# Kernel tuning notes

Measured on AMD Instinct MI355X. Metric: run time of the kernel, lower is better.

## Reference

```python
import jax, jax.numpy as jnp
import numpy as np

N = 4096
STD = 0.01


def setup_inputs() -> dict:
    key = jax.random.key(0)
    ks = jax.random.split(key, 16)
    p = lambda k, shape: STD * jax.random.normal(k, shape, dtype=jnp.float32)
    return {
        "t": 0,
        "x": jax.random.normal(ks[0], (N, 1), dtype=jnp.float32),
        "A": jax.random.normal(ks[1], (N, N), dtype=jnp.float32),
        # MLP_A: 2 -> 16 -> 16 -> 1 (ReLU between hidden layers), torch (out,in) layout
        "WA0": p(ks[2], (16, 2)), "bA0": p(ks[3], (16,)),
        "WA1": p(ks[4], (16, 16)), "bA1": p(ks[5], (16,)),
        "WA2": p(ks[6], (1, 16)), "bA2": p(ks[7], (1,)),
        # MLP: 1 -> 16 -> 1 (ReLU after first layer)
        "Wm0": p(ks[8], (16, 1)), "bm0": p(ks[9], (16,)),
        "Wm1": p(ks[10], (1, 16)), "bm1": p(ks[11], (1,)),
        # linear_A: 2 -> 1, no bias; linear_f: 1 -> 1, no bias
        "wA": p(ks[12], (1, 2)),
        "wf": p(ks[13], (1, 1)),
    }


def reference(t, x, A, WA0, bA0, WA1, bA1, WA2, bA2, Wm0, bm0, Wm1, bm1, wA, wf):
    n = x.shape[0]
    # node MLP branch: hidden_list[0] == 1 != 0
    x_N = jax.nn.relu(x @ Wm0.T + bm0) @ Wm1.T + bm1 + x @ wf.T  # (n, 1)
    # all-pairs features: x_a[i, j] = (x_i, x_j)
    x1 = jnp.broadcast_to(x, (n, n))       # row i = x_i repeated
    x2 = jnp.broadcast_to(x.T, (n, n))     # row i = full x vector
    x_a = jnp.stack((x1, x2), axis=-1)     # (n, n, 2)
    # edge MLP (2 -> 16 -> 16 -> 1) + skip linear_A (2 -> 1)
    h = jax.nn.relu(x_a @ WA0.T + bA0)     # (n, n, 16)
    h = jax.nn.relu(h @ WA1.T + bA1)       # (n, n, 16)
    x_e = (h @ WA2.T + bA2)[..., 0]        # (n, n)
    x_12 = (x_a @ wA.T)[..., 0]            # (n, n)
    # adjacency-weighted reduction over neighbors (dim=1)
    x_A = jnp.sum(A * (x_e + x_12), axis=1, keepdims=True)  # (n, 1)
    return x_N + x_A
```

## Files before the change

kernel.cpp:

```cpp
#include <hip/hip_runtime.h>
#include <hip/hip_bf16.h>


#define NN 4096

typedef __attribute__((ext_vector_type(8)))  short short8;
typedef __attribute__((ext_vector_type(2)))  float f32x2;
typedef __attribute__((ext_vector_type(16))) float f32x16;

__device__ __forceinline__ unsigned bf16_rne(float f) {
    unsigned u = __float_as_uint(f);
    return (u + 0x7fffu + ((u >> 16) & 1u)) >> 16;
}

__global__ __launch_bounds__(256, 4) void odef_kernel(
    const float* __restrict__ x,  const float* __restrict__ A,
    const float* __restrict__ WA0, const float* __restrict__ bA0,
    const float* __restrict__ WA1, const float* __restrict__ bA1,
    const float* __restrict__ WA2, const float* __restrict__ bA2,
    const float* __restrict__ Wm0, const float* __restrict__ bm0,
    const float* __restrict__ Wm1, const float* __restrict__ bm1,
    const float* __restrict__ wA,  const float* __restrict__ wf,
    float* __restrict__ out)
{
    __shared__ float partial[4];

    const int tid  = threadIdx.x;
    const int wave = tid >> 6;
    const int lane = tid & 63;
    const int n    = lane & 31;
    const int half = lane >> 5;
    const int row  = blockIdx.x * 2 + (wave >> 1);
    const int jbase = (wave & 1) * (NN / 2);

    const float xi = x[row];

    short8 a_frag;
    {
        union { short8 s8; unsigned u[4]; } au;
        #pragma unroll
        for (int p = 0; p < 4; ++p) {
            float lo = 0.f, hi = 0.f;
            if (n < 16) {
                int k = half * 8 + p * 2;
                lo = WA1[n * 16 + k];
                hi = WA1[n * 16 + k + 1];
            }
            au.u[p] = bf16_rne(lo) | (bf16_rne(hi) << 16);
        }
        a_frag = au.s8;
    }

    f32x2 u2[4], w2[4];
    #pragma unroll
    for (int p = 0; p < 4; ++p) {
        int k0 = half * 8 + p * 2;
        u2[p] = (f32x2){ fmaf(WA0[2 * k0],     xi, bA0[k0]),
                         fmaf(WA0[2 * k0 + 2], xi, bA0[k0 + 1]) };
        w2[p] = (f32x2){ WA0[2 * k0 + 1], WA0[2 * k0 + 3] };
    }

    f32x2 wa2_2[4];
    f32x16 cbias;
    #pragma unroll
    for (int r = 0; r < 16; ++r) cbias[r] = 0.f;
    #pragma unroll
    for (int q = 0; q < 4; ++q) {
        int r0 = 2 * q, r1 = 2 * q + 1;
        int m0 = (r0 & 3) + 8 * (r0 >> 2) + 4 * half;
        int m1 = (r1 & 3) + 8 * (r1 >> 2) + 4 * half;
        wa2_2[q] = (f32x2){ WA2[m0], WA2[m1] };
        cbias[r0] = bA1[m0];
        cbias[r1] = bA1[m1];
    }

    const float wA1h = half ? 0.f : wA[1];
    const float c0h  = half ? 0.f : (bA2[0] + wA[0] * xi);
    const f32x2 zero2 = { 0.f, 0.f };

    const float* Arow = A + (size_t)row * NN + jbase;
    const float* xrow = x + jbase;

    float acc = 0.f;

    #pragma unroll 2
    for (int jj = 0; jj < NN / 2; jj += 32) {
        float xg  = xrow[jj + n];
        float aij = Arow[jj + n];
        f32x2 xg2 = { xg, xg };
        union { short8 s8; unsigned u[4]; } bu;
        #pragma unroll
        for (int p = 0; p < 4; ++p) {
            f32x2 h = __builtin_elementwise_fma(w2[p], xg2, u2[p]);
            h = __builtin_elementwise_max(h, zero2);
            bu.u[p] = __builtin_amdgcn_perm(__float_as_uint(h.y),
                                            __float_as_uint(h.x),
                                            0x07060302u);
        }
        f32x16 d = __builtin_amdgcn_mfma_f32_32x32x16_bf16(a_frag, bu.s8, cbias, 0, 0, 0);
        f32x2 pp = { fmaf(wA1h, xg, c0h), 0.f };
        #pragma unroll
        for (int q = 0; q < 4; ++q) {
            f32x2 dq = { d[2 * q], d[2 * q + 1] };
            dq = __builtin_elementwise_max(dq, zero2);
            pp = __builtin_elementwise_fma(wa2_2[q], dq, pp);
        }
        acc = fmaf(aij, pp.x + pp.y, acc);
    }

    #pragma unroll
    for (int off = 32; off > 0; off >>= 1)
        acc += __shfl_xor(acc, off);
    if (lane == 0) partial[wave] = acc;
    __syncthreads();

    if (lane == 0 && (wave & 1) == 0) {
        float xn = fmaf(wf[0], xi, bm1[0]);
        #pragma unroll
        for (int h = 0; h < 16; ++h)
            xn = fmaf(Wm1[h], fmaxf(fmaf(Wm0[h], xi, bm0[h]), 0.f), xn);
        out[row] = xn + partial[wave] + partial[wave + 1];
    }
}

extern "C" void kernel_launch(void* const* d_in, const int* in_sizes, int n_in,
                              void* d_out, int out_size, void* d_ws, size_t ws_size,
                              hipStream_t stream) {
    const float* x   = (const float*)d_in[1];
    const float* A   = (const float*)d_in[2];
    const float* WA0 = (const float*)d_in[3];
    const float* bA0 = (const float*)d_in[4];
    const float* WA1 = (const float*)d_in[5];
    const float* bA1 = (const float*)d_in[6];
    const float* WA2 = (const float*)d_in[7];
    const float* bA2 = (const float*)d_in[8];
    const float* Wm0 = (const float*)d_in[9];
    const float* bm0 = (const float*)d_in[10];
    const float* Wm1 = (const float*)d_in[11];
    const float* bm1 = (const float*)d_in[12];
    const float* wA  = (const float*)d_in[13];
    const float* wf  = (const float*)d_in[14];
    float* out = (float*)d_out;

    odef_kernel<<<NN / 2, 256, 0, stream>>>(x, A, WA0, bA0, WA1, bA1, WA2, bA2,
                                            Wm0, bm0, Wm1, bm1, wA, wf, out);
}
```

Before: 168.9 us.

## Software-pipeline A and x loads with register double buffering and packed FMA asm

Result: faster. 163.4 us (-3.3%).

```diff
diff --git a/kernel.cpp b/kernel.cpp
--- a/kernel.cpp
+++ b/kernel.cpp
@@ -11,6 +11,15 @@
 __device__ __forceinline__ unsigned bf16_rne(float f) {
     unsigned u = __float_as_uint(f);
     return (u + 0x7fffu + ((u >> 16) & 1u)) >> 16;
+}
+
+__device__ __forceinline__ f32x2 pk_fma(f32x2 a, f32x2 b, f32x2 c) {
+    f32x2 d;
+    asm("v_pk_fma_f32 %0, %1, %2, %3" : "=v"(d) : "v"(a), "v"(b), "v"(c));
+    return d;
+}
+__device__ __forceinline__ f32x2 relu2(f32x2 a) {
+    return (f32x2){ fmaxf(a.x, 0.f), fmaxf(a.y, 0.f) };
 }
 
 __global__ __launch_bounds__(256, 4) void odef_kernel(
@@ -76,36 +85,49 @@
 
     const float wA1h = half ? 0.f : wA[1];
     const float c0h  = half ? 0.f : (bA2[0] + wA[0] * xi);
-    const f32x2 zero2 = { 0.f, 0.f };
 
     const float* Arow = A + (size_t)row * NN + jbase;
     const float* xrow = x + jbase;
 
     float acc = 0.f;
 
-    #pragma unroll 2
-    for (int jj = 0; jj < NN / 2; jj += 32) {
-        float xg  = xrow[jj + n];
-        float aij = Arow[jj + n];
-        f32x2 xg2 = { xg, xg };
-        union { short8 s8; unsigned u[4]; } bu;
+    float xb[2][8], ab[2][8];
+    #pragma unroll
+    for (int g = 0; g < 8; ++g) {
+        xb[0][g] = xrow[g * 32 + n];
+        ab[0][g] = Arow[g * 32 + n];
+    }
+
+    #pragma unroll
+    for (int m = 0; m < 8; ++m) {
+        const int cb = m & 1, nb = cb ^ 1;
+        const int mn = (m < 7) ? m + 1 : 7;
         #pragma unroll
-        for (int p = 0; p < 4; ++p) {
-            f32x2 h = __builtin_elementwise_fma(w2[p], xg2, u2[p]);
-            h = __builtin_elementwise_max(h, zero2);
-            bu.u[p] = __builtin_amdgcn_perm(__float_as_uint(h.y),
-                                            __float_as_uint(h.x),
-                                            0x07060302u);
+        for (int g = 0; g < 8; ++g) {
+            xb[nb][g] = xrow[mn * 256 + g * 32 + n];
+            ab[nb][g] = Arow[mn * 256 + g * 32 + n];
         }
-        f32x16 d = __builtin_amdgcn_mfma_f32_32x32x16_bf16(a_frag, bu.s8, cbias, 0, 0, 0);
-        f32x2 pp = { fmaf(wA1h, xg, c0h), 0.f };
         #pragma unroll
-        for (int q = 0; q < 4; ++q) {
-            f32x2 dq = { d[2 * q], d[2 * q + 1] };
-            dq = __builtin_elementwise_max(dq, zero2);
-            pp = __builtin_elementwise_fma(wa2_2[q], dq, pp);
+        for (int g = 0; g < 8; ++g) {
+            float xg  = xb[cb][g];
+            float aij = ab[cb][g];
+            f32x2 xg2 = { xg, xg };
+            union { short8 s8; unsigned u[4]; } bu;
+            #pragma unroll
+            for (int p = 0; p < 4; ++p) {
+                f32x2 h = relu2(pk_fma(w2[p], xg2, u2[p]));
+                bu.u[p] = __builtin_amdgcn_perm(__float_as_uint(h.y),
+                                                __float_as_uint(h.x),
+                                                0x07060302u);
+            }
+            union { f32x16 v16; f32x2 v2[8]; } du;
+            du.v16 = __builtin_amdgcn_mfma_f32_32x32x16_bf16(a_frag, bu.s8, cbias, 0, 0, 0);
+            f32x2 pp = { fmaf(wA1h, xg, c0h), 0.f };
+            #pragma unroll
+            for (int q = 0; q < 4; ++q)
+                pp = pk_fma(wa2_2[q], relu2(du.v2[q]), pp);
+            acc = fmaf(aij, pp.x + pp.y, acc);
         }
-        acc = fmaf(aij, pp.x + pp.y, acc);
     }
 
     #pragma unroll
```

## Switch edge MLP to fp16 packed math and prefetch inputs two iterations ahead

Applied to the files above, without the earlier changes.

Result: faster. 157.4 us (-6.8%).

```diff
diff --git a/kernel.cpp b/kernel.cpp
--- a/kernel.cpp
+++ b/kernel.cpp
@@ -4,13 +4,12 @@
 
 #define NN 4096
 
-typedef __attribute__((ext_vector_type(8)))  short short8;
-typedef __attribute__((ext_vector_type(2)))  float f32x2;
+typedef __fp16 half8  __attribute__((ext_vector_type(8)));
+typedef __fp16 half2v __attribute__((ext_vector_type(2)));
 typedef __attribute__((ext_vector_type(16))) float f32x16;
 
-__device__ __forceinline__ unsigned bf16_rne(float f) {
-    unsigned u = __float_as_uint(f);
-    return (u + 0x7fffu + ((u >> 16) & 1u)) >> 16;
+__device__ __forceinline__ half2v cvt2(float lo, float hi) {
+    return __builtin_amdgcn_cvt_pkrtz(lo, hi);
 }
 
 __global__ __launch_bounds__(256, 4) void odef_kernel(
@@ -35,77 +34,73 @@
 
     const float xi = x[row];
 
-    short8 a_frag;
-    {
-        union { short8 s8; unsigned u[4]; } au;
-        #pragma unroll
-        for (int p = 0; p < 4; ++p) {
-            float lo = 0.f, hi = 0.f;
-            if (n < 16) {
-                int k = half * 8 + p * 2;
-                lo = WA1[n * 16 + k];
-                hi = WA1[n * 16 + k + 1];
-            }
-            au.u[p] = bf16_rne(lo) | (bf16_rne(hi) << 16);
+    union { half2v h2[4]; half8 h8; } au;
+    #pragma unroll
+    for (int p = 0; p < 4; ++p) {
+        float lo = 0.f, hi = 0.f;
+        if (n < 16) {
+            int k = half * 8 + p * 2;
+            lo = WA1[n * 16 + k];
+            hi = WA1[n * 16 + k + 1];
         }
-        a_frag = au.s8;
+        au.h2[p] = cvt2(lo, hi);
     }
 
-    f32x2 u2[4], w2[4];
+    half2v u2h[4], w2h[4];
     #pragma unroll
     for (int p = 0; p < 4; ++p) {
         int k0 = half * 8 + p * 2;
-        u2[p] = (f32x2){ fmaf(WA0[2 * k0],     xi, bA0[k0]),
-                         fmaf(WA0[2 * k0 + 2], xi, bA0[k0 + 1]) };
-        w2[p] = (f32x2){ WA0[2 * k0 + 1], WA0[2 * k0 + 3] };
+        u2h[p] = cvt2(fmaf(WA0[2 * k0],     xi, bA0[k0]),
+                      fmaf(WA0[2 * k0 + 2], xi, bA0[k0 + 1]));
+        w2h[p] = cvt2(WA0[2 * k0 + 1], WA0[2 * k0 + 3]);
     }
 
-    f32x2 wa2_2[4];
+    float wa2s[8];
     f32x16 cbias;
     #pragma unroll
     for (int r = 0; r < 16; ++r) cbias[r] = 0.f;
     #pragma unroll
-    for (int q = 0; q < 4; ++q) {
-        int r0 = 2 * q, r1 = 2 * q + 1;
-        int m0 = (r0 & 3) + 8 * (r0 >> 2) + 4 * half;
-        int m1 = (r1 & 3) + 8 * (r1 >> 2) + 4 * half;
-        wa2_2[q] = (f32x2){ WA2[m0], WA2[m1] };
-        cbias[r0] = bA1[m0];
-        cbias[r1] = bA1[m1];
+    for (int r = 0; r < 8; ++r) {
+        int m = (r & 3) + 8 * (r >> 2) + 4 * half;
+        wa2s[r]  = WA2[m];
+        cbias[r] = bA1[m];
     }
 
     const float wA1h = half ? 0.f : wA[1];
     const float c0h  = half ? 0.f : (bA2[0] + wA[0] * xi);
-    const f32x2 zero2 = { 0.f, 0.f };
+    const half2v z2 = { (__fp16)0.f, (__fp16)0.f };
 
-    const float* Arow = A + (size_t)row * NN + jbase;
-    const float* xrow = x + jbase;
+    const float* xp = x + jbase;
+    const float* ap = A + (size_t)row * NN + jbase;
 
     float acc = 0.f;
 
-    #pragma unroll 2
-    for (int jj = 0; jj < NN / 2; jj += 32) {
-        float xg  = xrow[jj + n];
-        float aij = Arow[jj + n];
-        f32x2 xg2 = { xg, xg };
-        union { short8 s8; unsigned u[4]; } bu;
+    float xcur = xp[n],      acur = ap[n];
+    float xnxt = xp[32 + n], anxt = ap[32 + n];
+
+    #pragma unroll 4
+    for (int g = 0; g < 64; ++g) {
+        int gp = (g + 2 < 64) ? g + 2 : 63;
+        float xpre = xp[gp * 32 + n];
+        float apre = ap[gp * 32 + n];
+
+        half2v xgh = cvt2(xcur, xcur);
+        union { half2v h2[4]; half8 h8; } b;
         #pragma unroll
         for (int p = 0; p < 4; ++p) {
-            f32x2 h = __builtin_elementwise_fma(w2[p], xg2, u2[p]);
-            h = __builtin_elementwise_max(h, zero2);
-            bu.u[p] = __builtin_amdgcn_perm(__float_as_uint(h.y),
-                                            __float_as_uint(h.x),
-                                            0x07060302u);
+            half2v h = w2h[p] * xgh + u2h[p];
+            b.h2[p] = __builtin_elementwise_max(h, z2);
         }
-        f32x16 d = __builtin_amdgcn_mfma_f32_32x32x16_bf16(a_frag, bu.s8, cbias, 0, 0, 0);
-        f32x2 pp = { fmaf(wA1h, xg, c0h), 0.f };
+        f32x16 d = __builtin_amdgcn_mfma_f32_32x32x16_f16(au.h8, b.h8, cbias, 0, 0, 0);
+
+        float pp = fmaf(wA1h, xcur, c0h);
         #pragma unroll
-        for (int q = 0; q < 4; ++q) {
-            f32x2 dq = { d[2 * q], d[2 * q + 1] };
-            dq = __builtin_elementwise_max(dq, zero2);
-            pp = __builtin_elementwise_fma(wa2_2[q], dq, pp);
-        }
-        acc = fmaf(aij, pp.x + pp.y, acc);
+        for (int r = 0; r < 8; ++r)
+            pp = fmaf(wa2s[r], fmaxf(d[r], 0.f), pp);
+        acc = fmaf(acur, pp, acc);
+
+        xcur = xnxt; acur = anxt;
+        xnxt = xpre; anxt = apre;
     }
 
     #pragma unroll
```
